# Performance work log

Hardware: AMD Instinct MI355X
Metric: run time of the kernel (lower is better)

## Reference

```python
import jax, jax.numpy as jnp
import numpy as np
from jax import lax

CL, IL = 128, 64            # context_length, inst_length (globals in original)
PC, CH1, CH2, CH3 = 64, 128, 256, 256
CK1 = CK2 = CK3 = 3
F1, OUT = 400, 1
B = 4096
C3_OUT = CH3 * (CL - 1 - CK1 - CK2 - CK3 + 3)   # 256*121 = 30976
F1_IN = C3_OUT + CL * IL                        # 39168


def _uni(k, shape, fan_in):
    s = 1.0 / np.sqrt(fan_in)
    return jax.random.uniform(k, shape, jnp.float32, -s, s)


def setup_inputs() -> dict:
    key = jax.random.key(0)
    ks = jax.random.split(key, 14)
    x = jax.random.normal(ks[0], (B, CL * IL), jnp.float32)
    Wp = _uni(ks[1], (PC, IL, 2), IL * 2); bp = _uni(ks[2], (PC,), IL * 2)
    W1 = _uni(ks[3], (CH1, PC, CK1), PC * CK1); b1 = _uni(ks[4], (CH1,), PC * CK1)
    W2 = _uni(ks[5], (CH2, CH1, CK2), CH1 * CK2); b2 = _uni(ks[6], (CH2,), CH1 * CK2)
    W3 = _uni(ks[7], (CH3, CH2, CK3), CH2 * CK3); b3 = _uni(ks[8], (CH3,), CH2 * CK3)
    Wf1 = _uni(ks[9], (F1, F1_IN), F1_IN); bf1 = _uni(ks[10], (F1,), F1_IN)
    Wf2 = _uni(ks[11], (OUT, F1), F1); bf2 = _uni(ks[12], (OUT,), F1)
    return dict(x=x, Wp=Wp, bp=bp, W1=W1, b1=b1, W2=W2, b2=b2,
                W3=W3, b3=b3, Wf1=Wf1, bf1=bf1, Wf2=Wf2, bf2=bf2)


def _conv1d(h, w, b):
    # h: [B,C,L], w: [O,C,K], valid conv, stride 1
    return lax.conv_general_dilated(h, w, (1,), 'VALID',
                                    dimension_numbers=('NCH', 'OIH', 'NCH')) + b[None, :, None]


def reference(x, Wp, bp, W1, b1, W2, b2, W3, b3, Wf1, bf1, Wf2, bf2):
    b = x.shape[0]
    xt = x.reshape(b, CL, IL).transpose(0, 2, 1)          # [B, IL, CL]
    # Fused pairwise convp: original loops i=1..CL-1 over k=2 Conv1d on
    # (x[:,:,0], x[:,:,i]); equivalent to one shared term + one batched matmul.
    base = jnp.einsum('pc,bc->bp', Wp[:, :, 0], xt[:, :, 0])        # [B, PC]
    rest = jnp.einsum('pc,bci->bpi', Wp[:, :, 1], xt[:, :, 1:])     # [B, PC, CL-1]
    h = jax.nn.relu(base[:, :, None] + rest + bp[None, :, None])
    h = jax.nn.relu(_conv1d(h, W1, b1))
    h = jax.nn.relu(_conv1d(h, W2, b2))
    h = jax.nn.relu(_conv1d(h, W3, b3))
    h = h.reshape(b, C3_OUT)
    h = jnp.concatenate([h, xt.reshape(b, IL * CL)], axis=1)        # [B, F1_IN]
    h = jax.nn.relu(h @ Wf1.T + bf1)
    return h @ Wf2.T + bf2
```

## Files before the change

kernel.cpp:

```cpp
#include <hip/hip_runtime.h>


typedef __attribute__((ext_vector_type(8))) short bf16x8;
typedef __attribute__((ext_vector_type(4))) float f32x4;
typedef __attribute__((ext_vector_type(8))) unsigned short u16x8;
typedef __attribute__((ext_vector_type(4))) unsigned short u16x4;

#define DEVINL __device__ __forceinline__

DEVINL unsigned short f2bf(float f) {
  unsigned u = __builtin_bit_cast(unsigned, f);
  return (unsigned short)((u + 0x7fffu + ((u >> 16) & 1u)) >> 16);
}
DEVINL float bf2f(unsigned short h) {
  return __builtin_bit_cast(float, ((unsigned)h) << 16);
}
DEVINL f32x4 mfma16(bf16x8 a, bf16x8 b, f32x4 c) {
  return __builtin_amdgcn_mfma_f32_16x16x32_bf16(a, b, c, 0, 0, 0);
}
DEVINL float relu(float v) { return v > 0.f ? v : 0.f; }
DEVINL int sxg(int r, int c, int sh) {
  return (r << sh) + (((c >> 3) ^ (r & 7)) << 3) + (c & 7);
}

constexpr int NB = 4096;

__global__ __launch_bounds__(256) void k_prep_w(
    const float* __restrict__ Wp, const float* __restrict__ W1,
    const float* __restrict__ W2, const float* __restrict__ W3,
    unsigned short* __restrict__ wp1r, unsigned short* __restrict__ w1p,
    unsigned short* __restrict__ w2p, unsigned short* __restrict__ w3p) {
  int idx = blockIdx.x * 256 + threadIdx.x;
  if (idx < 4096) {
    int p = idx >> 6, i = idx & 63;
    wp1r[idx] = f2bf(Wp[(p * 64 + i) * 2 + 1]);
    return;
  }
  idx -= 4096;
  if (idx < 24576) {
    int f = idx >> 9, l = (idx >> 3) & 63, e = idx & 7;
    int mt = f & 7, t = f >> 3, ks = t & 1, k = t >> 1;
    int o = mt * 16 + (l & 15), c = ks * 32 + (l >> 4) * 8 + e;
    w1p[idx] = f2bf(W1[(o * 64 + c) * 3 + k]);
    return;
  }
  idx -= 24576;
  if (idx < 98304) {
    int f = idx >> 9, l = (idx >> 3) & 63, e = idx & 7;
    int mt = f & 15, t = f >> 4, ks = t & 3, k = t >> 2;
    int o = mt * 16 + (l & 15), c = ks * 32 + (l >> 4) * 8 + e;
    w2p[idx] = f2bf(W2[(o * 128 + c) * 3 + k]);
    return;
  }
  idx -= 98304;
  if (idx < 196608) {
    int f = idx >> 9, l = (idx >> 3) & 63, e = idx & 7;
    int mt = f & 15, t = f >> 4, ks = t & 7, k = t >> 3;
    int o = mt * 16 + (l & 15), c = ks * 32 + (l >> 4) * 8 + e;
    w3p[idx] = f2bf(W3[(o * 256 + c) * 3 + k]);
  }
}

__global__ __launch_bounds__(256) void k_prep_wf1(const float* __restrict__ wf1,
                                                  unsigned short* __restrict__ wf1r) {
  extern __shared__ unsigned short tls[];
  const int m = blockIdx.x, tid = threadIdx.x;
  const float* src = wf1 + (size_t)m * 39168;
  unsigned short* dst = wf1r + (size_t)m * 39168;
  for (int idx = tid; idx < 30976; idx += 256) {
    int o = idx / 121, l = idx - o * 121;
    tls[o * 130 + l] = f2bf(src[idx]);
  }
  __syncthreads();
  for (int idx = tid; idx < 30976; idx += 256) {
    int l = idx >> 8, o = idx & 255;
    dst[idx] = tls[o * 130 + l];
  }
  __syncthreads();
  for (int idx = tid; idx < 8192; idx += 256) {
    int il = idx >> 7, cl = idx & 127;
    tls[cl * 66 + il] = f2bf(src[30976 + idx]);
  }
  __syncthreads();
  for (int idx = tid; idx < 8192; idx += 256) {
    int cl = idx >> 6, il = idx & 63;
    dst[30976 + idx] = tls[cl * 66 + il];
  }
}

template <int CIN, int COUT, int LIN, int LOUT, int SSHI, int SSHO, bool TOGLB>
DEVINL void conv16(const unsigned short* in_lds,
                   const unsigned short* __restrict__ wpack,
                   const float* __restrict__ bias, unsigned short* out_lds,
                   unsigned short* h3, int b, int lane, int wv) {
  constexpr int KS = CIN / 32;
  constexpr int MT = COUT / 16;
  constexpr int MPW = MT / 4;
  const int lr = lane & 15, lq = lane >> 4;
  const int wm = wv >> 1, wn = wv & 1;
  f32x4 acc[MPW][4];
#pragma unroll
  for (int mi = 0; mi < MPW; ++mi)
#pragma unroll
    for (int ni = 0; ni < 4; ++ni) acc[mi][ni] = (f32x4){0.f, 0.f, 0.f, 0.f};
#pragma unroll
  for (int k = 0; k < 3; ++k)
#pragma unroll
    for (int ks = 0; ks < KS; ++ks) {
      bf16x8 a[MPW];
#pragma unroll
      for (int mi = 0; mi < MPW; ++mi)
        a[mi] = *(const bf16x8*)(wpack +
                                 (((k * KS + ks) * MT + wm * MPW + mi) << 9) +
                                 lane * 8);
      const int col = ks * 32 + lq * 8;
#pragma unroll
      for (int ni = 0; ni < 4; ++ni) {
        int l = (wn * 4 + ni) * 16 + lr + k;
        if (l > LIN - 1) l = LIN - 1;
        bf16x8 bb = *(const bf16x8*)(in_lds + sxg(l, col, SSHI));
#pragma unroll
        for (int mi = 0; mi < MPW; ++mi) acc[mi][ni] = mfma16(a[mi], bb, acc[mi][ni]);
      }
    }
#pragma unroll
  for (int mi = 0; mi < MPW; ++mi) {
    const int o0 = (wm * MPW + mi) * 16 + lq * 4;
    const f32x4 bi = *(const f32x4*)(bias + o0);
#pragma unroll
    for (int ni = 0; ni < 4; ++ni) {
      const int l = (wn * 4 + ni) * 16 + lr;
      if (l < LOUT) {
        u16x4 pk;
#pragma unroll
        for (int r = 0; r < 4; ++r) pk[r] = f2bf(relu(acc[mi][ni][r] + bi[r]));
        if constexpr (TOGLB)
          *(u16x4*)(h3 + ((size_t)b * LOUT + l) * COUT + o0) = pk;
        else
          *(u16x4*)(out_lds + sxg(l, o0, SSHO)) = pk;
      }
    }
  }
}

__global__ __launch_bounds__(512) void k_front(
    const float* __restrict__ x, const float* __restrict__ Wp,
    const float* __restrict__ bp, const unsigned short* __restrict__ wp1r,
    const unsigned short* __restrict__ w1p, const float* __restrict__ b1,
    const unsigned short* __restrict__ w2p, const float* __restrict__ b2,
    const unsigned short* __restrict__ w3p, const float* __restrict__ b3,
    unsigned short* __restrict__ h3) {
  extern __shared__ unsigned short lds[];
  unsigned short* xs = lds;
  unsigned short* h1s = lds;
  unsigned short* h0s = lds + 16000;
  unsigned short* h2s = lds + 16000;
  __shared__ float pbase[8][64];
  __shared__ float basel[64];
  const int b = blockIdx.x, tid = threadIdx.x;
  const int lane = tid & 63, wv = tid >> 6, lq = lane >> 4, lr = lane & 15;
  const float* xb = x + (size_t)b * 8192;

  for (int idx = tid * 4; idx < 8192; idx += 2048) {
    f32x4 v = *(const f32x4*)(xb + idx);
    int c = idx >> 6, i = idx & 63;
    u16x4 pk;
#pragma unroll
    for (int r = 0; r < 4; ++r) pk[r] = f2bf(v[r]);
    *(u16x4*)(xs + sxg(c, i, 6)) = pk;
  }
  __syncthreads();

  {
    int p = tid & 63, q = tid >> 6;
    float s = 0.f;
#pragma unroll
    for (int t = 0; t < 8; ++t) {
      int i = q * 8 + t;
      s += Wp[(p * 64 + i) * 2] * bf2f(xs[i]);
    }
    pbase[q][p] = s;
  }
  __syncthreads();
  if (tid < 64) {
    float s = bp[tid];
#pragma unroll
    for (int q = 0; q < 8; ++q) s += pbase[q][tid];
    basel[tid] = s;
  }
  __syncthreads();

  {
    const int mt = wv & 3, nh = wv >> 2;
    f32x4 acc[4];
#pragma unroll
    for (int t = 0; t < 4; ++t) acc[t] = (f32x4){0.f, 0.f, 0.f, 0.f};
#pragma unroll
    for (int s = 0; s < 2; ++s) {
      bf16x8 a = *(const bf16x8*)(wp1r + (mt * 16 + lr) * 64 + s * 32 + lq * 8);
#pragma unroll
      for (int t = 0; t < 4; ++t) {
        int j = (nh * 4 + t) * 16 + lr;
        int row = j + 1 > 127 ? 127 : j + 1;
        bf16x8 bb = *(const bf16x8*)(xs + sxg(row, s * 32 + lq * 8, 6));
        acc[t] = mfma16(a, bb, acc[t]);
      }
    }
    const int m0 = mt * 16 + lq * 4;
    f32x4 bl;
#pragma unroll
    for (int r = 0; r < 4; ++r) bl[r] = basel[m0 + r];
#pragma unroll
    for (int t = 0; t < 4; ++t) {
      int j = (nh * 4 + t) * 16 + lr;
      if (j < 127) {
        u16x4 pk;
#pragma unroll
        for (int r = 0; r < 4; ++r) pk[r] = f2bf(relu(acc[t][r] + bl[r]));
        *(u16x4*)(h0s + sxg(j, m0, 6)) = pk;
      }
    }
  }
  __syncthreads();

  conv16<64, 128, 127, 125, 6, 7, false>(h0s, w1p, b1, h1s, nullptr, b, lane, wv);
  __syncthreads();
  conv16<128, 256, 125, 123, 7, 8, false>(h1s, w2p, b2, h2s, nullptr, b, lane, wv);
  __syncthreads();
  conv16<256, 256, 123, 121, 8, 0, true>(h2s, w3p, b3, nullptr, h3, b, lane, wv);
}

__global__ __launch_bounds__(512) void k_fc1(const unsigned short* __restrict__ h3,
                                             const float* __restrict__ x,
                                             const unsigned short* __restrict__ wf1r,
                                             float* __restrict__ fpart, int chunkN) {
  __shared__ unsigned short lB[128 * 64];
  const int tid = threadIdx.x;
  const int lane = tid & 63, wv = tid >> 6, lq = lane >> 4, lr = lane & 15;
  const int slice = blockIdx.x & 31;
  const int bbase = (blockIdx.x >> 5) * 128;
  const int c0 = slice * 19 + (slice < 4 ? slice : 4);
  const int c1 = c0 + 19 + (slice < 4 ? 1 : 0);

  f32x4 acc[3][8], acc24;
#pragma unroll
  for (int mi = 0; mi < 3; ++mi)
#pragma unroll
    for (int nt = 0; nt < 8; ++nt) acc[mi][nt] = (f32x4){0.f, 0.f, 0.f, 0.f};
  acc24 = (f32x4){0.f, 0.f, 0.f, 0.f};

  const size_t arow0 = (size_t)((3 * wv + 0) * 16 + lr) * 39168;
  const size_t arow1 = (size_t)((3 * wv + 1) * 16 + lr) * 39168;
  const size_t arow2 = (size_t)((3 * wv + 2) * 16 + lr) * 39168;
  const size_t arow24 = (size_t)(384 + lr) * 39168;

  for (int kc = c0; kc < c1; ++kc) {
    const int k0 = kc * 64;
#pragma unroll
    for (int t = 0; t < 2; ++t) {
      int idx = tid + t * 512;
      int n = idx >> 3, ch = idx & 7;
      int bb = bbase + n;
      u16x8 v;
      if (k0 < 30976) {
        v = *(const u16x8*)(h3 + (size_t)bb * 30976 + k0 + ch * 8);
      } else {
        const float* sxp = x + (size_t)bb * 8192 + (k0 - 30976) + ch * 8;
        f32x4 v0 = *(const f32x4*)sxp;
        f32x4 v1 = *(const f32x4*)(sxp + 4);
#pragma unroll
        for (int r = 0; r < 4; ++r) {
          v[r] = f2bf(v0[r]);
          v[4 + r] = f2bf(v1[r]);
        }
      }
      *(u16x8*)(lB + (n << 6) + ((ch ^ (n & 7)) << 3)) = v;
    }
    __syncthreads();

#pragma unroll
    for (int win = 0; win < 2; ++win) {
      const int koff = k0 + win * 32 + lq * 8;
      bf16x8 a0 = *(const bf16x8*)(wf1r + arow0 + koff);
      bf16x8 a1 = *(const bf16x8*)(wf1r + arow1 + koff);
      bf16x8 a2 = *(const bf16x8*)(wf1r + arow2 + koff);
      bf16x8 a24 = *(const bf16x8*)(wf1r + arow24 + koff);
      const int cloc = win * 32 + lq * 8;
#pragma unroll
      for (int nt = 0; nt < 8; ++nt) {
        const int n = nt * 16 + lr;
        bf16x8 bb = *(const bf16x8*)(lB + sxg(n, cloc, 6));
        acc[0][nt] = mfma16(a0, bb, acc[0][nt]);
        acc[1][nt] = mfma16(a1, bb, acc[1][nt]);
        acc[2][nt] = mfma16(a2, bb, acc[2][nt]);
      }
      {
        const int n = wv * 16 + lr;
        bf16x8 bb = *(const bf16x8*)(lB + sxg(n, cloc, 6));
        acc24 = mfma16(a24, bb, acc24);
      }
    }
    __syncthreads();
  }

#pragma unroll
  for (int mi = 0; mi < 3; ++mi) {
    const int m0 = (3 * wv + mi) * 16 + lq * 4;
#pragma unroll
    for (int nt = 0; nt < 8; ++nt) {
      const int bb = bbase + nt * 16 + lr;
      *(f32x4*)(fpart + ((size_t)slice * chunkN + bb) * 400 + m0) = acc[mi][nt];
    }
  }
  {
    const int bb = bbase + wv * 16 + lr;
    *(f32x4*)(fpart + ((size_t)slice * chunkN + bb) * 400 + 384 + lq * 4) = acc24;
  }
}

__global__ __launch_bounds__(256) void k_fc1red(const float* __restrict__ fpart,
                                                const float* __restrict__ bf1,
                                                float* __restrict__ fc, int chunkN) {
  int idx = blockIdx.x * 256 + threadIdx.x;
  if (idx >= chunkN * 400) return;
  int m = idx % 400;
  float s = bf1[m];
  size_t stride = (size_t)chunkN * 400;
#pragma unroll 8
  for (int sl = 0; sl < 32; ++sl) s += fpart[(size_t)sl * stride + idx];
  fc[idx] = relu(s);
}

__global__ __launch_bounds__(256) void k_fc2(const float* __restrict__ fc,
                                             const float* __restrict__ wf2,
                                             const float* __restrict__ bf2,
                                             float* __restrict__ out) {
  int b = blockIdx.x * 4 + (threadIdx.x >> 6);
  int lane = threadIdx.x & 63;
  float s = 0.f;
  for (int m = lane; m < 400; m += 64) s += fc[(size_t)b * 400 + m] * wf2[m];
#pragma unroll
  for (int off = 32; off > 0; off >>= 1) s += __shfl_down(s, off, 64);
  if (lane == 0) out[b] = s + bf2[0];
}

extern "C" void kernel_launch(void* const* d_in, const int* in_sizes, int n_in,
                              void* d_out, int out_size, void* d_ws, size_t ws_size,
                              hipStream_t stream) {
  const float* x = (const float*)d_in[0];
  const float* Wp = (const float*)d_in[1];
  const float* bp = (const float*)d_in[2];
  const float* W1 = (const float*)d_in[3];
  const float* b1 = (const float*)d_in[4];
  const float* W2 = (const float*)d_in[5];
  const float* b2 = (const float*)d_in[6];
  const float* W3 = (const float*)d_in[7];
  const float* b3 = (const float*)d_in[8];
  const float* Wf1 = (const float*)d_in[9];
  const float* bf1 = (const float*)d_in[10];
  const float* Wf2 = (const float*)d_in[11];
  const float* bf2 = (const float*)d_in[12];
  float* out = (float*)d_out;

  static const int cand[4] = {4, 8, 16, 32};
  const size_t fixed = 8192 + 49152 + 196608 + 393216 + 31334400ULL;
  int nchunk = 32;
  for (int i = 0; i < 4; ++i) {
    size_t cn = NB / cand[i];
    size_t need = fixed + cn * 61952ULL + 32ULL * cn * 1600ULL + cn * 1600ULL;
    if (need <= ws_size) {
      nchunk = cand[i];
      break;
    }
  }
  const int chunkN = NB / nchunk;

  char* ws = (char*)d_ws;
  size_t off = 0;
  unsigned short* h3c = (unsigned short*)(ws + off);
  off += (size_t)chunkN * 61952ULL;
  float* fpart = (float*)(ws + off);
  off += 32ULL * chunkN * 1600ULL;
  float* fc = (float*)(ws + off);
  off += (size_t)chunkN * 1600ULL;
  unsigned short* wp1r = (unsigned short*)(ws + off);
  off += 8192;
  unsigned short* w1p = (unsigned short*)(ws + off);
  off += 49152;
  unsigned short* w2p = (unsigned short*)(ws + off);
  off += 196608;
  unsigned short* w3p = (unsigned short*)(ws + off);
  off += 393216;
  unsigned short* wf1r = (unsigned short*)(ws + off);

  k_prep_w<<<1264, 256, 0, stream>>>(Wp, W1, W2, W3, wp1r, w1p, w2p, w3p);
  k_prep_wf1<<<400, 256, 66560, stream>>>(Wf1, wf1r);

  for (int c = 0; c < nchunk; ++c) {
    const float* xc = x + (size_t)c * chunkN * 8192;
    k_front<<<chunkN, 512, 94976, stream>>>(xc, Wp, bp, wp1r, w1p, b1, w2p, b2,
                                            w3p, b3, h3c);
    k_fc1<<<(chunkN / 128) * 32, 512, 0, stream>>>(h3c, xc, wf1r, fpart, chunkN);
    k_fc1red<<<(chunkN * 400 + 255) / 256, 256, 0, stream>>>(fpart, bf1, fc, chunkN);
    k_fc2<<<chunkN / 4, 256, 0, stream>>>(fc, Wf2, bf2, out + (size_t)c * chunkN);
  }
}
```

Measured before the change: 770.6 us.

## Restructure fc1 tiling through LDS and split conv front into halves for occupancy

Rewrites the fc1 GEMM to stage weight tiles (padded to 448 rows) and activation tiles in LDS with a 7x4 MFMA tile per wave and a configurable K-split, instead of reading weights straight from global memory. The conv front end is split so conv2/conv3 run on two halves of the sequence, which shrinks LDS use and lets more blocks fit per CU (launch bounds now request 4). Weight prep is parallelized over more blocks, and Wp's first tap is pre-transposed to bf16. The workspace chunk and split selection changes too, trading more conv2 work and extra partial-sum traffic for better reuse and occupancy.

```diff
diff --git a/kernel.cpp b/kernel.cpp
--- a/kernel.cpp
+++ b/kernel.cpp
@@ -28,12 +28,14 @@
 __global__ __launch_bounds__(256) void k_prep_w(
     const float* __restrict__ Wp, const float* __restrict__ W1,
     const float* __restrict__ W2, const float* __restrict__ W3,
-    unsigned short* __restrict__ wp1r, unsigned short* __restrict__ w1p,
-    unsigned short* __restrict__ w2p, unsigned short* __restrict__ w3p) {
+    unsigned short* __restrict__ wp1r, unsigned short* __restrict__ wp0r,
+    unsigned short* __restrict__ w1p, unsigned short* __restrict__ w2p,
+    unsigned short* __restrict__ w3p) {
   int idx = blockIdx.x * 256 + threadIdx.x;
   if (idx < 4096) {
     int p = idx >> 6, i = idx & 63;
-    wp1r[idx] = f2bf(Wp[(p * 64 + i) * 2 + 1]);
+    wp1r[p * 64 + i] = f2bf(Wp[(p * 64 + i) * 2 + 1]);
+    wp0r[i * 64 + p] = f2bf(Wp[(p * 64 + i) * 2 + 0]);
     return;
   }
   idx -= 4096;
@@ -64,45 +66,60 @@
 __global__ __launch_bounds__(256) void k_prep_wf1(const float* __restrict__ wf1,
                                                   unsigned short* __restrict__ wf1r) {
   extern __shared__ unsigned short tls[];
-  const int m = blockIdx.x, tid = threadIdx.x;
-  const float* src = wf1 + (size_t)m * 39168;
+  const int m = blockIdx.x / 5, q = blockIdx.x % 5, tid = threadIdx.x;
   unsigned short* dst = wf1r + (size_t)m * 39168;
-  for (int idx = tid; idx < 30976; idx += 256) {
-    int o = idx / 121, l = idx - o * 121;
-    tls[o * 130 + l] = f2bf(src[idx]);
-  }
-  __syncthreads();
-  for (int idx = tid; idx < 30976; idx += 256) {
-    int l = idx >> 8, o = idx & 255;
-    dst[idx] = tls[o * 130 + l];
-  }
-  __syncthreads();
-  for (int idx = tid; idx < 8192; idx += 256) {
-    int il = idx >> 7, cl = idx & 127;
-    tls[cl * 66 + il] = f2bf(src[30976 + idx]);
-  }
-  __syncthreads();
-  for (int idx = tid; idx < 8192; idx += 256) {
-    int cl = idx >> 6, il = idx & 63;
-    dst[30976 + idx] = tls[cl * 66 + il];
-  }
-}
-
-template <int CIN, int COUT, int LIN, int LOUT, int SSHI, int SSHO, bool TOGLB>
-DEVINL void conv16(const unsigned short* in_lds,
-                   const unsigned short* __restrict__ wpack,
-                   const float* __restrict__ bias, unsigned short* out_lds,
-                   unsigned short* h3, int b, int lane, int wv) {
+  if (m >= 400) {
+    if (q < 4) {
+      for (int idx = tid; idx < 7744; idx += 256) dst[q * 7744 + idx] = 0;
+    } else {
+      for (int idx = tid; idx < 8192; idx += 256) dst[30976 + idx] = 0;
+    }
+    return;
+  }
+  if (q < 4) {
+    const float* src = wf1 + (size_t)m * 39168 + q * 7744;
+    for (int idx = tid; idx < 7744; idx += 256) {
+      int o = idx / 121, l = idx - o * 121;
+      tls[o * 132 + l] = f2bf(src[idx]);
+    }
+    __syncthreads();
+    for (int idx = tid; idx < 7744; idx += 256) {
+      int l = idx >> 6, o = idx & 63;
+      dst[l * 256 + q * 64 + o] = tls[o * 132 + l];
+    }
+  } else {
+    const float* src = wf1 + (size_t)m * 39168 + 30976;
+    for (int idx = tid; idx < 8192; idx += 256) {
+      int il = idx >> 7, cl = idx & 127;
+      tls[cl * 66 + il] = f2bf(src[idx]);
+    }
+    __syncthreads();
+    for (int idx = tid; idx < 8192; idx += 256) {
+      int cl = idx >> 6, il = idx & 63;
+      dst[30976 + idx] = tls[cl * 66 + il];
+    }
+  }
+}
+
+template <int CIN, int COUT, int SSHI, int SSHO, int MPW, int NPW, bool TOGLB>
+DEVINL void conv_phase(const unsigned short* in_lds,
+                       const unsigned short* __restrict__ wpack,
+                       const float* __restrict__ bias,
+                       unsigned short* out_lds, unsigned short* h3, int b,
+                       int lane, int wv, int rowoff, int rowclamp, int outbase,
+                       int outvalid) {
   constexpr int KS = CIN / 32;
   constexpr int MT = COUT / 16;
-  constexpr int MPW = MT / 4;
+  constexpr int GM = MT / MPW;
+  constexpr int GN = 8 / GM;
+  static_assert(GM * GN == 8, "");
   const int lr = lane & 15, lq = lane >> 4;
-  const int wm = wv >> 1, wn = wv & 1;
-  f32x4 acc[MPW][4];
+  const int wm = wv / GN, wn = wv % GN;
+  f32x4 acc[MPW][NPW];
 #pragma unroll
   for (int mi = 0; mi < MPW; ++mi)
 #pragma unroll
-    for (int ni = 0; ni < 4; ++ni) acc[mi][ni] = (f32x4){0.f, 0.f, 0.f, 0.f};
+    for (int ni = 0; ni < NPW; ++ni) acc[mi][ni] = (f32x4){0.f, 0.f, 0.f, 0.f};
 #pragma unroll
   for (int k = 0; k < 3; ++k)
 #pragma unroll
@@ -115,12 +132,13 @@
                                  lane * 8);
       const int col = ks * 32 + lq * 8;
 #pragma unroll
-      for (int ni = 0; ni < 4; ++ni) {
-        int l = (wn * 4 + ni) * 16 + lr + k;
-        if (l > LIN - 1) l = LIN - 1;
-        bf16x8 bb = *(const bf16x8*)(in_lds + sxg(l, col, SSHI));
-#pragma unroll
-        for (int mi = 0; mi < MPW; ++mi) acc[mi][ni] = mfma16(a[mi], bb, acc[mi][ni]);
+      for (int ni = 0; ni < NPW; ++ni) {
+        int row = rowoff + (wn * NPW + ni) * 16 + lr + k;
+        if (row > rowclamp) row = rowclamp;
+        bf16x8 bb = *(const bf16x8*)(in_lds + sxg(row, col, SSHI));
+#pragma unroll
+        for (int mi = 0; mi < MPW; ++mi)
+          acc[mi][ni] = mfma16(a[mi], bb, acc[mi][ni]);
       }
     }
 #pragma unroll
@@ -128,23 +146,23 @@
     const int o0 = (wm * MPW + mi) * 16 + lq * 4;
     const f32x4 bi = *(const f32x4*)(bias + o0);
 #pragma unroll
-    for (int ni = 0; ni < 4; ++ni) {
-      const int l = (wn * 4 + ni) * 16 + lr;
-      if (l < LOUT) {
+    for (int ni = 0; ni < NPW; ++ni) {
+      const int ll = (wn * NPW + ni) * 16 + lr;
+      if (ll < outvalid) {
         u16x4 pk;
 #pragma unroll
         for (int r = 0; r < 4; ++r) pk[r] = f2bf(relu(acc[mi][ni][r] + bi[r]));
         if constexpr (TOGLB)
-          *(u16x4*)(h3 + ((size_t)b * LOUT + l) * COUT + o0) = pk;
+          *(u16x4*)(h3 + ((size_t)b * 121 + outbase + ll) * 256 + o0) = pk;
         else
-          *(u16x4*)(out_lds + sxg(l, o0, SSHO)) = pk;
-      }
-    }
-  }
-}
-
-__global__ __launch_bounds__(512) void k_front(
-    const float* __restrict__ x, const float* __restrict__ Wp,
+          *(u16x4*)(out_lds + sxg(ll, o0, SSHO)) = pk;
+      }
+    }
+  }
+}
+
+__global__ __launch_bounds__(512, 4) void k_front(
+    const float* __restrict__ x, const unsigned short* __restrict__ wp0r,
     const float* __restrict__ bp, const unsigned short* __restrict__ wp1r,
     const unsigned short* __restrict__ w1p, const float* __restrict__ b1,
     const unsigned short* __restrict__ w2p, const float* __restrict__ b2,
@@ -152,9 +170,9 @@
     unsigned short* __restrict__ h3) {
   extern __shared__ unsigned short lds[];
   unsigned short* xs = lds;
-  unsigned short* h1s = lds;
-  unsigned short* h0s = lds + 16000;
-  unsigned short* h2s = lds + 16000;
+  unsigned short* h0s = lds + 8192;
+  unsigned short* h2h = lds;
+  unsigned short* h1s = lds + 16384;
   __shared__ float pbase[8][64];
   __shared__ float basel[64];
   const int b = blockIdx.x, tid = threadIdx.x;
@@ -177,7 +195,7 @@
 #pragma unroll
     for (int t = 0; t < 8; ++t) {
       int i = q * 8 + t;
-      s += Wp[(p * 64 + i) * 2] * bf2f(xs[i]);
+      s += bf2f(wp0r[i * 64 + p]) * bf2f(xs[i]);
     }
     pbase[q][p] = s;
   }
@@ -223,43 +241,56 @@
   }
   __syncthreads();
 
-  conv16<64, 128, 127, 125, 6, 7, false>(h0s, w1p, b1, h1s, nullptr, b, lane, wv);
-  __syncthreads();
-  conv16<128, 256, 125, 123, 7, 8, false>(h1s, w2p, b2, h2s, nullptr, b, lane, wv);
-  __syncthreads();
-  conv16<256, 256, 123, 121, 8, 0, true>(h2s, w3p, b3, nullptr, h3, b, lane, wv);
-}
-
-__global__ __launch_bounds__(512) void k_fc1(const unsigned short* __restrict__ h3,
-                                             const float* __restrict__ x,
-                                             const unsigned short* __restrict__ wf1r,
-                                             float* __restrict__ fpart, int chunkN) {
-  __shared__ unsigned short lB[128 * 64];
+  conv_phase<64, 128, 6, 7, 2, 4, false>(h0s, w1p, b1, h1s, nullptr, b, lane,
+                                         wv, 0, 126, 0, 125);
+  __syncthreads();
+  conv_phase<128, 256, 7, 8, 4, 2, false>(h1s, w2p, b2, h2h, nullptr, b, lane,
+                                          wv, 0, 124, 0, 64);
+  __syncthreads();
+  conv_phase<256, 256, 8, 0, 2, 4, true>(h2h, w3p, b3, nullptr, h3, b, lane,
+                                         wv, 0, 63, 0, 62);
+  __syncthreads();
+  conv_phase<128, 256, 7, 8, 4, 2, false>(h1s, w2p, b2, h2h, nullptr, b, lane,
+                                          wv, 62, 124, 0, 61);
+  __syncthreads();
+  conv_phase<256, 256, 8, 0, 2, 4, true>(h2h, w3p, b3, nullptr, h3, b, lane,
+                                         wv, 0, 63, 62, 59);
+}
+
+__global__ __launch_bounds__(512, 2) void k_fc1(
+    const unsigned short* __restrict__ h3, const float* __restrict__ x,
+    const unsigned short* __restrict__ wf1r, float* __restrict__ fpart,
+    int chunkN, int S) {
+  __shared__ unsigned short lA[448 * 40];
+  __shared__ unsigned short lB[128 * 40];
   const int tid = threadIdx.x;
   const int lane = tid & 63, wv = tid >> 6, lq = lane >> 4, lr = lane & 15;
-  const int slice = blockIdx.x & 31;
-  const int bbase = (blockIdx.x >> 5) * 128;
-  const int c0 = slice * 19 + (slice < 4 ? slice : 4);
-  const int c1 = c0 + 19 + (slice < 4 ? 1 : 0);
-
-  f32x4 acc[3][8], acc24;
-#pragma unroll
-  for (int mi = 0; mi < 3; ++mi)
-#pragma unroll
-    for (int nt = 0; nt < 8; ++nt) acc[mi][nt] = (f32x4){0.f, 0.f, 0.f, 0.f};
-  acc24 = (f32x4){0.f, 0.f, 0.f, 0.f};
-
-  const size_t arow0 = (size_t)((3 * wv + 0) * 16 + lr) * 39168;
-  const size_t arow1 = (size_t)((3 * wv + 1) * 16 + lr) * 39168;
-  const size_t arow2 = (size_t)((3 * wv + 2) * 16 + lr) * 39168;
-  const size_t arow24 = (size_t)(384 + lr) * 39168;
+  const int slice = blockIdx.x % S;
+  const int bbase = (blockIdx.x / S) * 128;
+  const int per = 1224 / S, rem = 1224 % S;
+  const int c0 = slice * per + (slice < rem ? slice : rem);
+  const int c1 = c0 + per + (slice < rem ? 1 : 0);
+  const int mgrp = wv >> 1, ngrp = wv & 1;
+
+  f32x4 acc[7][4];
+#pragma unroll
+  for (int mt = 0; mt < 7; ++mt)
+#pragma unroll
+    for (int ni = 0; ni < 4; ++ni) acc[mt][ni] = (f32x4){0.f, 0.f, 0.f, 0.f};
 
   for (int kc = c0; kc < c1; ++kc) {
-    const int k0 = kc * 64;
-#pragma unroll
-    for (int t = 0; t < 2; ++t) {
+    const int k0 = kc * 32;
+#pragma unroll
+    for (int t = 0; t < 4; ++t) {
       int idx = tid + t * 512;
-      int n = idx >> 3, ch = idx & 7;
+      if (idx < 1792) {
+        int m = idx >> 2, ch = idx & 3;
+        *(u16x8*)(lA + m * 40 + ch * 8) =
+            *(const u16x8*)(wf1r + (size_t)m * 39168 + k0 + ch * 8);
+      }
+    }
+    {
+      int n = tid >> 2, ch = tid & 3;
       int bb = bbase + n;
       u16x8 v;
       if (k0 < 30976) {
@@ -274,60 +305,45 @@
           v[4 + r] = f2bf(v1[r]);
         }
       }
-      *(u16x8*)(lB + (n << 6) + ((ch ^ (n & 7)) << 3)) = v;
+      *(u16x8*)(lB + n * 40 + ch * 8) = v;
     }
     __syncthreads();
-
-#pragma unroll
-    for (int win = 0; win < 2; ++win) {
-      const int koff = k0 + win * 32 + lq * 8;
-      bf16x8 a0 = *(const bf16x8*)(wf1r + arow0 + koff);
-      bf16x8 a1 = *(const bf16x8*)(wf1r + arow1 + koff);
-      bf16x8 a2 = *(const bf16x8*)(wf1r + arow2 + koff);
-      bf16x8 a24 = *(const bf16x8*)(wf1r + arow24 + koff);
-      const int cloc = win * 32 + lq * 8;
-#pragma unroll
-      for (int nt = 0; nt < 8; ++nt) {
-        const int n = nt * 16 + lr;
-        bf16x8 bb = *(const bf16x8*)(lB + sxg(n, cloc, 6));
-        acc[0][nt] = mfma16(a0, bb, acc[0][nt]);
-        acc[1][nt] = mfma16(a1, bb, acc[1][nt]);
-        acc[2][nt] = mfma16(a2, bb, acc[2][nt]);
-      }
-      {
-        const int n = wv * 16 + lr;
-        bf16x8 bb = *(const bf16x8*)(lB + sxg(n, cloc, 6));
-        acc24 = mfma16(a24, bb, acc24);
-      }
+    bf16x8 bfr[4];
+#pragma unroll
+    for (int ni = 0; ni < 4; ++ni)
+      bfr[ni] = *(const bf16x8*)(lB + (ngrp * 64 + ni * 16 + lr) * 40 + lq * 8);
+#pragma unroll
+    for (int mt = 0; mt < 7; ++mt) {
+      bf16x8 afr =
+          *(const bf16x8*)(lA + (mgrp * 112 + mt * 16 + lr) * 40 + lq * 8);
+#pragma unroll
+      for (int ni = 0; ni < 4; ++ni)
+        acc[mt][ni] = mfma16(afr, bfr[ni], acc[mt][ni]);
     }
     __syncthreads();
   }
 
 #pragma unroll
-  for (int mi = 0; mi < 3; ++mi) {
-    const int m0 = (3 * wv + mi) * 16 + lq * 4;
-#pragma unroll
-    for (int nt = 0; nt < 8; ++nt) {
-      const int bb = bbase + nt * 16 + lr;
-      *(f32x4*)(fpart + ((size_t)slice * chunkN + bb) * 400 + m0) = acc[mi][nt];
-    }
-  }
-  {
-    const int bb = bbase + wv * 16 + lr;
-    *(f32x4*)(fpart + ((size_t)slice * chunkN + bb) * 400 + 384 + lq * 4) = acc24;
+  for (int mt = 0; mt < 7; ++mt) {
+    const int m0 = mgrp * 112 + mt * 16 + lq * 4;
+#pragma unroll
+    for (int ni = 0; ni < 4; ++ni) {
+      const int bb = bbase + ngrp * 64 + ni * 16 + lr;
+      *(f32x4*)(fpart + ((size_t)slice * chunkN + bb) * 448 + m0) = acc[mt][ni];
+    }
   }
 }
 
 __global__ __launch_bounds__(256) void k_fc1red(const float* __restrict__ fpart,
                                                 const float* __restrict__ bf1,
-                                                float* __restrict__ fc, int chunkN) {
+                                                float* __restrict__ fc,
+                                                int chunkN, int S) {
   int idx = blockIdx.x * 256 + threadIdx.x;
   if (idx >= chunkN * 400) return;
-  int m = idx % 400;
+  int bq = idx / 400, m = idx - bq * 400;
   float s = bf1[m];
-  size_t stride = (size_t)chunkN * 400;
-#pragma unroll 8
-  for (int sl = 0; sl < 32; ++sl) s += fpart[(size_t)sl * stride + idx];
+  for (int sl = 0; sl < S; ++sl)
+    s += fpart[((size_t)sl * chunkN + bq) * 448 + m];
   fc[idx] = relu(s);
 }
 
@@ -362,28 +378,31 @@
   const float* bf2 = (const float*)d_in[12];
   float* out = (float*)d_out;
 
-  static const int cand[4] = {4, 8, 16, 32};
-  const size_t fixed = 8192 + 49152 + 196608 + 393216 + 31334400ULL;
-  int nchunk = 32;
+  const size_t fixed = 8192 + 8192 + 49152 + 196608 + 393216 + 448ULL * 39168 * 2;
+  static const int cand[4][2] = {{2048, 16}, {1024, 32}, {512, 64}, {512, 32}};
+  int chunkN = 512, S = 32;
   for (int i = 0; i < 4; ++i) {
-    size_t cn = NB / cand[i];
-    size_t need = fixed + cn * 61952ULL + 32ULL * cn * 1600ULL + cn * 1600ULL;
+    size_t cn = cand[i][0], s = cand[i][1];
+    size_t need = fixed + cn * (61952ULL + 1600ULL) + s * cn * 1792ULL;
     if (need <= ws_size) {
-      nchunk = cand[i];
+      chunkN = cand[i][0];
+      S = cand[i][1];
       break;
     }
   }
-  const int chunkN = NB / nchunk;
+  const int nchunk = NB / chunkN;
 
   char* ws = (char*)d_ws;
   size_t off = 0;
   unsigned short* h3c = (unsigned short*)(ws + off);
   off += (size_t)chunkN * 61952ULL;
   float* fpart = (float*)(ws + off);
-  off += 32ULL * chunkN * 1600ULL;
+  off += (size_t)S * chunkN * 1792ULL;
   float* fc = (float*)(ws + off);
   off += (size_t)chunkN * 1600ULL;
   unsigned short* wp1r = (unsigned short*)(ws + off);
+  off += 8192;
+  unsigned short* wp0r = (unsigned short*)(ws + off);
   off += 8192;
   unsigned short* w1p = (unsigned short*)(ws + off);
   off += 49152;
@@ -393,15 +412,16 @@
   off += 393216;
   unsigned short* wf1r = (unsigned short*)(ws + off);
 
-  k_prep_w<<<1264, 256, 0, stream>>>(Wp, W1, W2, W3, wp1r, w1p, w2p, w3p);
-  k_prep_wf1<<<400, 256, 66560, stream>>>(Wf1, wf1r);
+  k_prep_w<<<1264, 256, 0, stream>>>(Wp, W1, W2, W3, wp1r, wp0r, w1p, w2p, w3p);
+  k_prep_wf1<<<448 * 5, 256, 16896, stream>>>(Wf1, wf1r);
 
   for (int c = 0; c < nchunk; ++c) {
     const float* xc = x + (size_t)c * chunkN * 8192;
-    k_front<<<chunkN, 512, 94976, stream>>>(xc, Wp, bp, wp1r, w1p, b1, w2p, b2,
-                                            w3p, b3, h3c);
-    k_fc1<<<(chunkN / 128) * 32, 512, 0, stream>>>(h3c, xc, wf1r, fpart, chunkN);
-    k_fc1red<<<(chunkN * 400 + 255) / 256, 256, 0, stream>>>(fpart, bf1, fc, chunkN);
+    k_front<<<chunkN, 512, 64768, stream>>>(xc, wp0r, bp, wp1r, w1p, b1, w2p,
+                                            b2, w3p, b3, h3c);
+    k_fc1<<<(chunkN / 128) * S, 512, 0, stream>>>(h3c, xc, wf1r, fpart, chunkN, S);
+    k_fc1red<<<(chunkN * 400 + 255) / 256, 256, 0, stream>>>(fpart, bf1, fc,
+                                                             chunkN, S);
     k_fc2<<<chunkN / 4, 256, 0, stream>>>(fc, Wf2, bf2, out + (size_t)c * chunkN);
   }
 }
```

Measured after the change: 1.227 ms. 1.59x slower.

## Double-buffer fc1 LDS tiles, reduce K-split slices, split Wf1 prep across blocks

Applied to the files above, without the earlier changes.

The fc1 kernel now double-buffers its LDS B tile: the global load for the next K chunk is issued before the MFMAs on the current chunk, and each iteration ends with one barrier instead of two sync points. The K split drops from 32 slices to a runtime S=16, which roughly halves the partial-sum traffic in the reduction. Chunk size is now picked from {2048,1024,512} rows, so there are fewer launch iterations. Wf1 preparation runs over 2000 smaller blocks with less shared memory, and Wp's first tap is pre-transposed to bf16 for coalesced reads in k_front. The tradeoffs are fewer fc1 blocks per chunk, which may lower occupancy and parallelism, and extra registers for the prefetch.

```diff
diff --git a/kernel.cpp b/kernel.cpp
--- a/kernel.cpp
+++ b/kernel.cpp
@@ -28,12 +28,14 @@
 __global__ __launch_bounds__(256) void k_prep_w(
     const float* __restrict__ Wp, const float* __restrict__ W1,
     const float* __restrict__ W2, const float* __restrict__ W3,
-    unsigned short* __restrict__ wp1r, unsigned short* __restrict__ w1p,
-    unsigned short* __restrict__ w2p, unsigned short* __restrict__ w3p) {
+    unsigned short* __restrict__ wp1r, unsigned short* __restrict__ wp0r,
+    unsigned short* __restrict__ w1p, unsigned short* __restrict__ w2p,
+    unsigned short* __restrict__ w3p) {
   int idx = blockIdx.x * 256 + threadIdx.x;
   if (idx < 4096) {
     int p = idx >> 6, i = idx & 63;
-    wp1r[idx] = f2bf(Wp[(p * 64 + i) * 2 + 1]);
+    wp1r[p * 64 + i] = f2bf(Wp[(p * 64 + i) * 2 + 1]);
+    wp0r[i * 64 + p] = f2bf(Wp[(p * 64 + i) * 2 + 0]);
     return;
   }
   idx -= 4096;
@@ -64,27 +66,30 @@
 __global__ __launch_bounds__(256) void k_prep_wf1(const float* __restrict__ wf1,
                                                   unsigned short* __restrict__ wf1r) {
   extern __shared__ unsigned short tls[];
-  const int m = blockIdx.x, tid = threadIdx.x;
-  const float* src = wf1 + (size_t)m * 39168;
+  const int m = blockIdx.x / 5, q = blockIdx.x % 5, tid = threadIdx.x;
   unsigned short* dst = wf1r + (size_t)m * 39168;
-  for (int idx = tid; idx < 30976; idx += 256) {
-    int o = idx / 121, l = idx - o * 121;
-    tls[o * 130 + l] = f2bf(src[idx]);
-  }
-  __syncthreads();
-  for (int idx = tid; idx < 30976; idx += 256) {
-    int l = idx >> 8, o = idx & 255;
-    dst[idx] = tls[o * 130 + l];
-  }
-  __syncthreads();
-  for (int idx = tid; idx < 8192; idx += 256) {
-    int il = idx >> 7, cl = idx & 127;
-    tls[cl * 66 + il] = f2bf(src[30976 + idx]);
-  }
-  __syncthreads();
-  for (int idx = tid; idx < 8192; idx += 256) {
-    int cl = idx >> 6, il = idx & 63;
-    dst[30976 + idx] = tls[cl * 66 + il];
+  if (q < 4) {
+    const float* src = wf1 + (size_t)m * 39168 + q * 7744;
+    for (int idx = tid; idx < 7744; idx += 256) {
+      int o = idx / 121, l = idx - o * 121;
+      tls[o * 132 + l] = f2bf(src[idx]);
+    }
+    __syncthreads();
+    for (int idx = tid; idx < 7744; idx += 256) {
+      int l = idx >> 6, o = idx & 63;
+      dst[l * 256 + q * 64 + o] = tls[o * 132 + l];
+    }
+  } else {
+    const float* src = wf1 + (size_t)m * 39168 + 30976;
+    for (int idx = tid; idx < 8192; idx += 256) {
+      int il = idx >> 7, cl = idx & 127;
+      tls[cl * 66 + il] = f2bf(src[idx]);
+    }
+    __syncthreads();
+    for (int idx = tid; idx < 8192; idx += 256) {
+      int cl = idx >> 6, il = idx & 63;
+      dst[30976 + idx] = tls[cl * 66 + il];
+    }
   }
 }
 
@@ -120,7 +125,8 @@
         if (l > LIN - 1) l = LIN - 1;
         bf16x8 bb = *(const bf16x8*)(in_lds + sxg(l, col, SSHI));
 #pragma unroll
-        for (int mi = 0; mi < MPW; ++mi) acc[mi][ni] = mfma16(a[mi], bb, acc[mi][ni]);
+        for (int mi = 0; mi < MPW; ++mi)
+          acc[mi][ni] = mfma16(a[mi], bb, acc[mi][ni]);
       }
     }
 #pragma unroll
@@ -144,7 +150,7 @@
 }
 
 __global__ __launch_bounds__(512) void k_front(
-    const float* __restrict__ x, const float* __restrict__ Wp,
+    const float* __restrict__ x, const unsigned short* __restrict__ wp0r,
     const float* __restrict__ bp, const unsigned short* __restrict__ wp1r,
     const unsigned short* __restrict__ w1p, const float* __restrict__ b1,
     const unsigned short* __restrict__ w2p, const float* __restrict__ b2,
@@ -177,7 +183,7 @@
 #pragma unroll
     for (int t = 0; t < 8; ++t) {
       int i = q * 8 + t;
-      s += Wp[(p * 64 + i) * 2] * bf2f(xs[i]);
+      s += bf2f(wp0r[i * 64 + p]) * bf2f(xs[i]);
     }
     pbase[q][p] = s;
   }
@@ -233,14 +239,16 @@
 __global__ __launch_bounds__(512) void k_fc1(const unsigned short* __restrict__ h3,
                                              const float* __restrict__ x,
                                              const unsigned short* __restrict__ wf1r,
-                                             float* __restrict__ fpart, int chunkN) {
-  __shared__ unsigned short lB[128 * 64];
+                                             float* __restrict__ fpart,
+                                             int chunkN, int S) {
+  __shared__ unsigned short lB[2][128 * 64];
   const int tid = threadIdx.x;
   const int lane = tid & 63, wv = tid >> 6, lq = lane >> 4, lr = lane & 15;
-  const int slice = blockIdx.x & 31;
-  const int bbase = (blockIdx.x >> 5) * 128;
-  const int c0 = slice * 19 + (slice < 4 ? slice : 4);
-  const int c1 = c0 + 19 + (slice < 4 ? 1 : 0);
+  const int slice = blockIdx.x % S;
+  const int bbase = (blockIdx.x / S) * 128;
+  const int per = 612 / S, rem = 612 % S;
+  const int c0 = slice * per + (slice < rem ? slice : rem);
+  const int c1 = c0 + per + (slice < rem ? 1 : 0);
 
   f32x4 acc[3][8], acc24;
 #pragma unroll
@@ -254,54 +262,88 @@
   const size_t arow2 = (size_t)((3 * wv + 2) * 16 + lr) * 39168;
   const size_t arow24 = (size_t)(384 + lr) * 39168;
 
+  const int sn0 = tid >> 3, sch0 = tid & 7;
+  const int sn1 = (tid + 512) >> 3, sch1 = tid & 7;
+  const unsigned short* hrow0 = h3 + (size_t)(bbase + sn0) * 30976 + sch0 * 8;
+  const unsigned short* hrow1 = h3 + (size_t)(bbase + sn1) * 30976 + sch1 * 8;
+  const float* xrow0 = x + (size_t)(bbase + sn0) * 8192 + sch0 * 8;
+  const float* xrow1 = x + (size_t)(bbase + sn1) * 8192 + sch1 * 8;
+  const int woff0 = (sn0 << 6) + ((sch0 ^ (sn0 & 7)) << 3);
+  const int woff1 = (sn1 << 6) + ((sch1 ^ (sn1 & 7)) << 3);
+
+  u16x8 hv0, hv1;
+  f32x4 xv00, xv01, xv10, xv11;
+  bool isx;
+
+#define FC1_GLOAD(KC)                                                     \
+  {                                                                       \
+    const int k0_ = (KC)*64;                                              \
+    isx = (k0_ >= 30976);                                                 \
+    if (!isx) {                                                           \
+      hv0 = *(const u16x8*)(hrow0 + k0_);                                 \
+      hv1 = *(const u16x8*)(hrow1 + k0_);                                 \
+    } else {                                                              \
+      xv00 = *(const f32x4*)(xrow0 + (k0_ - 30976));                      \
+      xv01 = *(const f32x4*)(xrow0 + (k0_ - 30976) + 4);                  \
+      xv10 = *(const f32x4*)(xrow1 + (k0_ - 30976));                      \
+      xv11 = *(const f32x4*)(xrow1 + (k0_ - 30976) + 4);                  \
+    }                                                                     \
+  }
+#define FC1_DSWRITE(BUF)                                                  \
+  {                                                                       \
+    if (isx) {                                                            \
+      _Pragma("unroll") for (int r = 0; r < 4; ++r) {                     \
+        hv0[r] = f2bf(xv00[r]);                                           \
+        hv0[4 + r] = f2bf(xv01[r]);                                       \
+        hv1[r] = f2bf(xv10[r]);                                           \
+        hv1[4 + r] = f2bf(xv11[r]);                                       \
+      }                                                                   \
+    }                                                                     \
+    *(u16x8*)(lB[BUF] + woff0) = hv0;                                     \
+    *(u16x8*)(lB[BUF] + woff1) = hv1;                                     \
+  }
+
+  FC1_GLOAD(c0)
+  FC1_DSWRITE(0)
+  __syncthreads();
+
   for (int kc = c0; kc < c1; ++kc) {
+    const int p = (kc - c0) & 1;
     const int k0 = kc * 64;
-#pragma unroll
-    for (int t = 0; t < 2; ++t) {
-      int idx = tid + t * 512;
-      int n = idx >> 3, ch = idx & 7;
-      int bb = bbase + n;
-      u16x8 v;
-      if (k0 < 30976) {
-        v = *(const u16x8*)(h3 + (size_t)bb * 30976 + k0 + ch * 8);
-      } else {
-        const float* sxp = x + (size_t)bb * 8192 + (k0 - 30976) + ch * 8;
-        f32x4 v0 = *(const f32x4*)sxp;
-        f32x4 v1 = *(const f32x4*)(sxp + 4);
-#pragma unroll
-        for (int r = 0; r < 4; ++r) {
-          v[r] = f2bf(v0[r]);
-          v[4 + r] = f2bf(v1[r]);
-        }
-      }
-      *(u16x8*)(lB + (n << 6) + ((ch ^ (n & 7)) << 3)) = v;
-    }
-    __syncthreads();
-
+    const bool more = (kc + 1 < c1);
+    if (more) FC1_GLOAD(kc + 1)
+
+    bf16x8 aP[2][4];
 #pragma unroll
     for (int win = 0; win < 2; ++win) {
       const int koff = k0 + win * 32 + lq * 8;
-      bf16x8 a0 = *(const bf16x8*)(wf1r + arow0 + koff);
-      bf16x8 a1 = *(const bf16x8*)(wf1r + arow1 + koff);
-      bf16x8 a2 = *(const bf16x8*)(wf1r + arow2 + koff);
-      bf16x8 a24 = *(const bf16x8*)(wf1r + arow24 + koff);
+      aP[win][0] = *(const bf16x8*)(wf1r + arow0 + koff);
+      aP[win][1] = *(const bf16x8*)(wf1r + arow1 + koff);
+      aP[win][2] = *(const bf16x8*)(wf1r + arow2 + koff);
+      aP[win][3] = *(const bf16x8*)(wf1r + arow24 + koff);
+    }
+#pragma unroll
+    for (int win = 0; win < 2; ++win) {
       const int cloc = win * 32 + lq * 8;
 #pragma unroll
       for (int nt = 0; nt < 8; ++nt) {
         const int n = nt * 16 + lr;
-        bf16x8 bb = *(const bf16x8*)(lB + sxg(n, cloc, 6));
-        acc[0][nt] = mfma16(a0, bb, acc[0][nt]);
-        acc[1][nt] = mfma16(a1, bb, acc[1][nt]);
-        acc[2][nt] = mfma16(a2, bb, acc[2][nt]);
+        bf16x8 bb = *(const bf16x8*)(lB[p] + sxg(n, cloc, 6));
+        acc[0][nt] = mfma16(aP[win][0], bb, acc[0][nt]);
+        acc[1][nt] = mfma16(aP[win][1], bb, acc[1][nt]);
+        acc[2][nt] = mfma16(aP[win][2], bb, acc[2][nt]);
       }
       {
         const int n = wv * 16 + lr;
-        bf16x8 bb = *(const bf16x8*)(lB + sxg(n, cloc, 6));
-        acc24 = mfma16(a24, bb, acc24);
-      }
-    }
+        bf16x8 bb = *(const bf16x8*)(lB[p] + sxg(n, cloc, 6));
+        acc24 = mfma16(aP[win][3], bb, acc24);
+      }
+    }
+    if (more) FC1_DSWRITE(p ^ 1)
     __syncthreads();
   }
+#undef FC1_GLOAD
+#undef FC1_DSWRITE
 
 #pragma unroll
   for (int mi = 0; mi < 3; ++mi) {
@@ -320,14 +362,15 @@
 
 __global__ __launch_bounds__(256) void k_fc1red(const float* __restrict__ fpart,
                                                 const float* __restrict__ bf1,
-                                                float* __restrict__ fc, int chunkN) {
+                                                float* __restrict__ fc,
+                                                int chunkN, int S) {
   int idx = blockIdx.x * 256 + threadIdx.x;
   if (idx >= chunkN * 400) return;
   int m = idx % 400;
   float s = bf1[m];
   size_t stride = (size_t)chunkN * 400;
-#pragma unroll 8
-  for (int sl = 0; sl < 32; ++sl) s += fpart[(size_t)sl * stride + idx];
+#pragma unroll 4
+  for (int sl = 0; sl < S; ++sl) s += fpart[(size_t)sl * stride + idx];
   fc[idx] = relu(s);
 }
 
@@ -362,28 +405,32 @@
   const float* bf2 = (const float*)d_in[12];
   float* out = (float*)d_out;
 
-  static const int cand[4] = {4, 8, 16, 32};
-  const size_t fixed = 8192 + 49152 + 196608 + 393216 + 31334400ULL;
-  int nchunk = 32;
-  for (int i = 0; i < 4; ++i) {
-    size_t cn = NB / cand[i];
-    size_t need = fixed + cn * 61952ULL + 32ULL * cn * 1600ULL + cn * 1600ULL;
+  const size_t fixed =
+      8192 + 8192 + 49152 + 196608 + 393216 + 400ULL * 39168 * 2;
+  const int S = 16;
+  static const int cand[3] = {2048, 1024, 512};
+  int chunkN = 512;
+  for (int i = 0; i < 3; ++i) {
+    size_t cn = cand[i];
+    size_t need = fixed + cn * 61952ULL + (size_t)S * cn * 1600ULL + cn * 1600ULL;
     if (need <= ws_size) {
-      nchunk = cand[i];
+      chunkN = cand[i];
       break;
     }
   }
-  const int chunkN = NB / nchunk;
+  const int nchunk = NB / chunkN;
 
   char* ws = (char*)d_ws;
   size_t off = 0;
   unsigned short* h3c = (unsigned short*)(ws + off);
   off += (size_t)chunkN * 61952ULL;
   float* fpart = (float*)(ws + off);
-  off += 32ULL * chunkN * 1600ULL;
+  off += (size_t)S * chunkN * 1600ULL;
   float* fc = (float*)(ws + off);
   off += (size_t)chunkN * 1600ULL;
   unsigned short* wp1r = (unsigned short*)(ws + off);
+  off += 8192;
+  unsigned short* wp0r = (unsigned short*)(ws + off);
   off += 8192;
   unsigned short* w1p = (unsigned short*)(ws + off);
   off += 49152;
@@ -393,15 +440,16 @@
   off += 393216;
   unsigned short* wf1r = (unsigned short*)(ws + off);
 
-  k_prep_w<<<1264, 256, 0, stream>>>(Wp, W1, W2, W3, wp1r, w1p, w2p, w3p);
-  k_prep_wf1<<<400, 256, 66560, stream>>>(Wf1, wf1r);
+  k_prep_w<<<1264, 256, 0, stream>>>(Wp, W1, W2, W3, wp1r, wp0r, w1p, w2p, w3p);
+  k_prep_wf1<<<2000, 256, 16896, stream>>>(Wf1, wf1r);
 
   for (int c = 0; c < nchunk; ++c) {
     const float* xc = x + (size_t)c * chunkN * 8192;
-    k_front<<<chunkN, 512, 94976, stream>>>(xc, Wp, bp, wp1r, w1p, b1, w2p, b2,
-                                            w3p, b3, h3c);
-    k_fc1<<<(chunkN / 128) * 32, 512, 0, stream>>>(h3c, xc, wf1r, fpart, chunkN);
-    k_fc1red<<<(chunkN * 400 + 255) / 256, 256, 0, stream>>>(fpart, bf1, fc, chunkN);
+    k_front<<<chunkN, 512, 94976, stream>>>(xc, wp0r, bp, wp1r, w1p, b1, w2p,
+                                            b2, w3p, b3, h3c);
+    k_fc1<<<(chunkN / 128) * S, 512, 0, stream>>>(h3c, xc, wf1r, fpart, chunkN, S);
+    k_fc1red<<<(chunkN * 400 + 255) / 256, 256, 0, stream>>>(fpart, bf1, fc,
+                                                             chunkN, S);
     k_fc2<<<chunkN / 4, 256, 0, stream>>>(fc, Wf2, bf2, out + (size_t)c * chunkN);
   }
 }
```

Result: faster. 693.9 us (-10.0%).
